# Optimization experiments

Hardware: AMD Instinct MI355X
Metric: run time of the kernel (lower is better)

The kernel has to match this reference:

```python
import jax, jax.numpy as jnp
import numpy as np

N = 50000      # nodes
E = 800000     # edges (before self loops)
H = 4          # heads
C = 32         # hidden_channels per head
HC = H * C     # 128
L = 3          # num_layers - 2 conv blocks
G = 128        # graphs in batch
OUT = 10       # out_channels
VOCAB = 100
EPS = 1e-5


def setup_inputs() -> dict:
    key = jax.random.key(0)
    ks = jax.random.split(key, 16)
    s = 0.1
    return {
        "x_idx": jax.random.randint(ks[0], (N,), 0, VOCAB),
        "edge_index": jax.random.randint(ks[1], (2, E), 0, N),
        "batch": jnp.sort(jax.random.randint(ks[2], (N,), 0, G)),
        "embed": jax.random.normal(ks[3], (VOCAB, HC), jnp.float32) * s,
        "bn_gamma": jnp.ones((L, HC), jnp.float32),
        "bn_beta": jnp.zeros((L, HC), jnp.float32),
        "lin_W": jax.random.normal(ks[4], (L, C, HC), jnp.float32) * s,   # maps HC -> C (hidden)
        "lin_b": jnp.zeros((L, C), jnp.float32),
        "gat_W": jax.random.normal(ks[5], (L, HC, C), jnp.float32) * s,   # maps C -> H*C
        "att_src": jax.random.normal(ks[6], (L, H, C), jnp.float32) * s,
        "att_dst": jax.random.normal(ks[7], (L, H, C), jnp.float32) * s,
        "gat_b": jnp.zeros((L, HC), jnp.float32),
        "readout_W": jax.random.normal(ks[8], (OUT, HC), jnp.float32) * s,
        "readout_b": jnp.zeros((OUT,), jnp.float32),
    }


def _segment_softmax(logits, seg, num_segments):
    # logits: [E, H], seg: [E]
    m = jax.ops.segment_max(logits, seg, num_segments=num_segments)
    m = jnp.where(jnp.isfinite(m), m, 0.0)
    e = jnp.exp(logits - m[seg])
    z = jax.ops.segment_sum(e, seg, num_segments=num_segments)
    return e / (z[seg] + 1e-16)


def _forward(x_idx, edge_index, batch, embed, bn_gamma, bn_beta, lin_W, lin_b,
             gat_W, att_src, att_dst, gat_b, readout_W, readout_b):
    x = embed[x_idx]                                   # [N, HC]
    loops = jnp.arange(N)
    src = jnp.concatenate([edge_index[0], loops])      # add_self_loops=True
    dst = jnp.concatenate([edge_index[1], loops])
    for l in range(L):
        # BatchNorm1d (batch statistics)
        mean = jnp.mean(x, axis=0)
        var = jnp.var(x, axis=0)
        x = bn_gamma[l] * (x - mean) * jax.lax.rsqrt(var + EPS) + bn_beta[l]
        # Linear(HC -> C) + relu; dropout = identity (eval)
        x = jax.nn.relu(x @ lin_W[l].T + lin_b[l])      # [N, C]
        # GATConv(C -> C, heads=H, concat)
        h = (x @ gat_W[l].T).reshape(N, H, C)           # [N, H, C]
        a_src = jnp.sum(h * att_src[l], axis=-1)        # [N, H]
        a_dst = jnp.sum(h * att_dst[l], axis=-1)        # [N, H]
        logits = jax.nn.leaky_relu(a_src[src] + a_dst[dst], 0.2)  # [E+N, H]
        alpha = _segment_softmax(logits, dst, N)        # softmax over in-edges of each dst
        msg = h[src] * alpha[:, :, None]                # [E+N, H, C]
        x = jax.ops.segment_sum(msg, dst, num_segments=N).reshape(N, HC) + gat_b[l]
    x = x @ readout_W.T + readout_b                     # [N, OUT]
    return jax.ops.segment_sum(x, batch, num_segments=G)  # [G, OUT]


def reference(x_idx, edge_index, batch, embed, bn_gamma, bn_beta, lin_W, lin_b,
              gat_W, att_src, att_dst, gat_b, readout_W, readout_b):
    return _forward(x_idx, edge_index, batch, embed, bn_gamma, bn_beta, lin_W, lin_b,
                    gat_W, att_src, att_dst, gat_b, readout_W, readout_b)
```

## Files before the change

### kernel.cpp

```cpp
#include <hip/hip_runtime.h>

constexpr int NN   = 50000;
constexpr int NE   = 800000;
constexpr int NHD  = 4;
constexpr int CC   = 32;
constexpr int HCC  = 128;
constexpr int NL   = 3;
constexpr int NG   = 128;
constexpr int NOUT = 10;
constexpr float BN_EPS = 1e-5f;

constexpr int X2S = 67;
constexpr int YS = 33;
constexpr int NSLOT = 64;
constexpr int NBUK = (NN + 127) / 128;
constexpr int EB  = 8192;

__device__ inline unsigned f2bf_pack(float a, float b) {
    unsigned ua = __float_as_uint(a); ua += 0x7FFFu + ((ua >> 16) & 1u);
    unsigned ub = __float_as_uint(b); ub += 0x7FFFu + ((ub >> 16) & 1u);
    return (ua >> 16) | (ub & 0xFFFF0000u);
}
__device__ inline float bf_lo(unsigned p) { return __uint_as_float(p << 16); }
__device__ inline float bf_hi(unsigned p) { return __uint_as_float(p & 0xFFFF0000u); }

__global__ __launch_bounds__(256) void k_embed_stats(const int* __restrict__ idx,
                                                     const float* __restrict__ embed,
                                                     unsigned* __restrict__ xp,
                                                     float* __restrict__ stats) {
    int tid = threadIdx.x;
    int i0 = blockIdx.x * 256 + tid;
    int stride = gridDim.x * 256;
    float s0 = 0.f, s1 = 0.f, q0 = 0.f, q1 = 0.f;
    for (int i = i0; i < NN * 64; i += stride) {
        int n = i >> 6, c2 = (i & 63) << 1;
        float2 ev = *(const float2*)(embed + (size_t)idx[n] * HCC + c2);
        xp[i] = f2bf_pack(ev.x, ev.y);
        s0 += ev.x; q0 += ev.x * ev.x;
        s1 += ev.y; q1 += ev.y * ev.y;
    }
    __shared__ float A[256], B[256], C[256], D[256];
    A[tid] = s0; B[tid] = s1; C[tid] = q0; D[tid] = q1;
    __syncthreads();
    int slot = blockIdx.x & (NSLOT - 1);
    if (tid < 64) {
        int p = tid;
        float S0 = A[p] + A[p + 64] + A[p + 128] + A[p + 192];
        float S1 = B[p] + B[p + 64] + B[p + 128] + B[p + 192];
        float Q0 = C[p] + C[p + 64] + C[p + 128] + C[p + 192];
        float Q1 = D[p] + D[p + 64] + D[p + 128] + D[p + 192];
        atomicAdd(&stats[slot * 256 + 2 * p],           S0);
        atomicAdd(&stats[slot * 256 + 2 * p + 1],       S1);
        atomicAdd(&stats[slot * 256 + HCC + 2 * p],     Q0);
        atomicAdd(&stats[slot * 256 + HCC + 2 * p + 1], Q1);
    }
}

__global__ __launch_bounds__(256) void k_bhist(const int* __restrict__ ei,
                                               int* __restrict__ bkcnt,
                                               const int* __restrict__ batch,
                                               float* __restrict__ gcnt) {
    __shared__ int hist[NBUK];
    __shared__ int lgc[NG];
    int b = blockIdx.x, t = threadIdx.x;
    int e0 = b * EB, nE = min(EB, NE - e0);
    for (int i = t; i < NBUK; i += 256) hist[i] = 0;
    for (int i = t; i < NG; i += 256) lgc[i] = 0;
    __syncthreads();
    for (int i = t; i < nE; i += 256)
        atomicAdd(&hist[ei[NE + e0 + i] >> 7], 1);
    int n0 = b * 512;
    for (int i = t; i < 512; i += 256) {
        int n = n0 + i;
        if (n < NN) atomicAdd(&lgc[batch[n]], 1);
    }
    __syncthreads();
    for (int i = t; i < NBUK; i += 256)
        if (hist[i]) atomicAdd(&bkcnt[i], hist[i]);
    for (int i = t; i < NG; i += 256)
        if (lgc[i]) atomicAdd(&gcnt[i], (float)lgc[i]);
}

__global__ __launch_bounds__(512) void k_bscan(const int* __restrict__ bkcnt,
                                               int* __restrict__ bbase,
                                               int* __restrict__ bcnt,
                                               int* __restrict__ rowptr) {
    __shared__ int sc[512];
    int t = threadIdx.x;
    int v = (t < NBUK) ? bkcnt[t] : 0;
    sc[t] = v;
    __syncthreads();
#pragma unroll
    for (int off = 1; off < 512; off <<= 1) {
        int u = (t >= off) ? sc[t - off] : 0;
        __syncthreads();
        sc[t] += u;
        __syncthreads();
    }
    if (t < NBUK) {
        int excl = sc[t] - v;
        bbase[t] = excl;
        bcnt[t]  = excl;
    }
    if (t == 0) rowptr[NN] = NE;
}

__global__ __launch_bounds__(256) void k_bin(const int* __restrict__ ei,
                                             int* __restrict__ bcnt,
                                             unsigned* __restrict__ e_src) {
    __shared__ int hist[NBUK], base[NBUK];
    int b = blockIdx.x, t = threadIdx.x;
    int e0 = b * EB;
    int nE = min(EB, NE - e0);

    for (int i = t; i < NBUK; i += 256) hist[i] = 0;
    __syncthreads();
    for (int i = t; i < nE; i += 256)
        atomicAdd(&hist[ei[NE + e0 + i] >> 7], 1);
    __syncthreads();
    for (int i = t; i < NBUK; i += 256) {
        int c = hist[i];
        if (c) base[i] = atomicAdd(&bcnt[i], c);
        hist[i] = 0;
    }
    __syncthreads();
    for (int i = t; i < nE; i += 256) {
        int e = e0 + i;
        int d = ei[NE + e];
        int s = ei[e];
        int bk = d >> 7;
        int pos = base[bk] + atomicAdd(&hist[bk], 1);
        e_src[pos] = (unsigned)s | ((unsigned)(d & 127) << 17);
    }
}

__global__ __launch_bounds__(256) void k_place(const int* __restrict__ bbase,
                                               unsigned* __restrict__ e_src,
                                               int* __restrict__ rowptr) {
    __shared__ int lcnt[128], sc[128], lrp[128], cnt[128];
    int b = blockIdx.x, t = threadIdx.x;
    int d0 = b * 128;
    int rS = bbase[b];
    int rE = (b + 1 < NBUK) ? bbase[b + 1] : NE;
    int n = rE - rS;
    if (t < 128) { lcnt[t] = 0; cnt[t] = 0; }
    __syncthreads();
    unsigned pk[14];
#pragma unroll
    for (int k = 0; k < 14; k++) {
        int i = t + k * 256;
        if (i < n) {
            pk[k] = e_src[rS + i];
            atomicAdd(&lcnt[pk[k] >> 17], 1);
        }
    }
    __syncthreads();
    if (t < 128) sc[t] = lcnt[t];
    __syncthreads();
#pragma unroll
    for (int off = 1; off < 128; off <<= 1) {
        int u = (t < 128 && t >= off) ? sc[t - off] : 0;
        __syncthreads();
        if (t < 128) sc[t] += u;
        __syncthreads();
    }
    if (t < 128) {
        int start = rS + sc[t] - lcnt[t];
        lrp[t] = start;
        int d = d0 + t;
        if (d < NN) rowptr[d] = start;
    }
    __syncthreads();
#pragma unroll
    for (int k = 0; k < 14; k++) {
        int i = t + k * 256;
        if (i < n) {
            unsigned p = pk[k];
            int dl = p >> 17;
            int pos = lrp[dl] + atomicAdd(&cnt[dl], 1);
            e_src[pos] = p & 0x1FFFFu;
        }
    }
}

__global__ __launch_bounds__(256) void k_fused(const unsigned* __restrict__ xp,
                                               const float* __restrict__ stats,
                                               const float* __restrict__ gamma,
                                               const float* __restrict__ beta,
                                               const float* __restrict__ W1,
                                               const float* __restrict__ b1,
                                               const float* __restrict__ W2,
                                               const float* __restrict__ aS,
                                               const float* __restrict__ aD,
                                               unsigned* __restrict__ h,
                                               float* __restrict__ asrc,
                                               float* __restrict__ adst) {
    __shared__ unsigned xb2[64 * X2S];
    __shared__ float yt[64 * YS];
    __shared__ float __attribute__((aligned(16))) ssl[256];
    int tid = threadIdx.x;
    int node0 = blockIdx.x * 64;
    int nNodes = min(64, NN - node0);

    if (tid < 128) {
        float s = 0.f, q = 0.f;
        for (int sl = 0; sl < NSLOT; sl++) {
            s += stats[sl * 256 + tid];
            q += stats[sl * 256 + HCC + tid];
        }
        float mean = s * (1.0f / NN);
        float var  = q * (1.0f / NN) - mean * mean;
        float sc   = gamma[tid] * rsqrtf(var + BN_EPS);
        ssl[tid]       = sc;
        ssl[HCC + tid] = beta[tid] - mean * sc;
    }
    __syncthreads();

    {
        for (int q4 = tid; q4 < nNodes * 16; q4 += 256) {
            int n = q4 >> 4, c8 = q4 & 15;
            uint4 xv = *(const uint4*)(xp + (size_t)(node0 + n) * 64 + c8 * 4);
            int c = c8 * 8;
            float4 sc0 = *(const float4*)&ssl[c];
            float4 sc1 = *(const float4*)&ssl[c + 4];
            float4 sh0 = *(const float4*)&ssl[HCC + c];
            float4 sh1 = *(const float4*)&ssl[HCC + c + 4];
            unsigned* dst = &xb2[n * X2S + c8 * 4];
            dst[0] = f2bf_pack(bf_lo(xv.x) * sc0.x + sh0.x, bf_hi(xv.x) * sc0.y + sh0.y);
            dst[1] = f2bf_pack(bf_lo(xv.y) * sc0.z + sh0.z, bf_hi(xv.y) * sc0.w + sh0.w);
            dst[2] = f2bf_pack(bf_lo(xv.z) * sc1.x + sh1.x, bf_hi(xv.z) * sc1.y + sh1.y);
            dst[3] = f2bf_pack(bf_lo(xv.w) * sc1.z + sh1.z, bf_hi(xv.w) * sc1.w + sh1.w);
        }
    }
    __syncthreads();

    int lane = tid & 63;
    int wv = __builtin_amdgcn_readfirstlane(tid >> 6);
    int n = lane;

    {
        int j0 = wv * 8;
        const float* w1p = W1 + j0 * 128;
        float acc[8];
#pragma unroll
        for (int k = 0; k < 8; k++) acc[k] = b1[j0 + k];
        if (n < nNodes) {
            for (int cb = 0; cb < 128; cb += 4) {
                unsigned p0 = xb2[n * X2S + (cb >> 1)];
                unsigned p1 = xb2[n * X2S + (cb >> 1) + 1];
                float xv0 = bf_lo(p0), xv1 = bf_hi(p0);
                float xv2 = bf_lo(p1), xv3 = bf_hi(p1);
#pragma unroll
                for (int k = 0; k < 8; k++) {
                    float4 w = *(const float4*)&w1p[k * 128 + cb];
                    acc[k] += xv0 * w.x + xv1 * w.y + xv2 * w.z + xv3 * w.w;
                }
            }
#pragma unroll
            for (int k = 0; k < 8; k++) yt[n * YS + j0 + k] = fmaxf(acc[k], 0.f);
        }
    }
    __syncthreads();

    if (n < nNodes) {
        int k0 = wv * 32, hd = wv;
        const float* w2p = W2 + k0 * 32;
        const float* aSp = aS + hd * 32;
        const float* aDp = aD + hd * 32;
        float yreg[32];
#pragma unroll
        for (int j = 0; j < 32; j++) yreg[j] = yt[n * YS + j];
        float sa = 0.f, da = 0.f;
        unsigned* hrow = h + (size_t)(node0 + n) * 64;
        for (int kb = 0; kb < 32; kb += 8) {
            float acck[8];
#pragma unroll
            for (int kk = 0; kk < 8; kk++) acck[kk] = 0.f;
#pragma unroll
            for (int j = 0; j < 32; j += 4) {
#pragma unroll
                for (int kk = 0; kk < 8; kk++) {
                    float4 w = *(const float4*)&w2p[(kb + kk) * 32 + j];
                    acck[kk] += yreg[j] * w.x + yreg[j + 1] * w.y +
                                yreg[j + 2] * w.z + yreg[j + 3] * w.w;
                }
            }
#pragma unroll
            for (int kk = 0; kk < 8; kk++) {
                sa += acck[kk] * aSp[kb + kk];
                da += acck[kk] * aDp[kb + kk];
            }
            uint4 pk;
            pk.x = f2bf_pack(acck[0], acck[1]);
            pk.y = f2bf_pack(acck[2], acck[3]);
            pk.z = f2bf_pack(acck[4], acck[5]);
            pk.w = f2bf_pack(acck[6], acck[7]);
            *(uint4*)(hrow + ((kb) >> 1) + (k0 >> 1)) = pk;
        }
        asrc[(node0 + n) * 4 + hd] = sa;
        adst[(node0 + n) * 4 + hd] = da;
    }
}

__global__ __launch_bounds__(256) void k_agg(const int* __restrict__ rowptr,
                                             const int* __restrict__ e_src,
                                             const float* __restrict__ asrc,
                                             const float* __restrict__ adst,
                                             const unsigned* __restrict__ h,
                                             const float* __restrict__ gat_b,
                                             unsigned* __restrict__ xo,
                                             float* __restrict__ stats,
                                             const int* __restrict__ batch,
                                             float* __restrict__ gsum,
                                             int mode) {
    int tid = threadIdx.x, lane = tid & 63, wv = tid >> 6;
    int g  = lane >> 4;
    int li = lane & 15;
    int hd = li >> 2;
    int d  = blockIdx.x * 16 + wv * 4 + g;

    float4 bA = *(const float4*)(gat_b + li * 8);
    float4 bB = *(const float4*)(gat_b + li * 8 + 4);

    int begin = rowptr[d];
    int end   = rowptr[d + 1];
    float adv = adst[d * 4 + hd];
    float asl = asrc[d * 4 + hd];
    uint4 hs  = *(const uint4*)(h + (size_t)d * 64 + li * 4);

    float acc[8];
#pragma unroll
    for (int k = 0; k < 8; k++) acc[k] = 0.f;
    float ws = 0.f;

    int s[4];
    if (begin < end) {
#pragma unroll
        for (int t = 0; t < 4; t++) s[t] = e_src[min(begin + t, end - 1)];
    }

    for (int j = begin; j < end; j += 4) {
        uint4 hv[4];
#pragma unroll
        for (int t = 0; t < 4; t++) hv[t] = *(const uint4*)(h + (size_t)s[t] * 64 + li * 4);
        float av[4];
#pragma unroll
        for (int t = 0; t < 4; t++) av[t] = asrc[s[t] * 4 + hd];
        int jn = j + 4;
        int sn[4];
#pragma unroll
        for (int t = 0; t < 4; t++) sn[t] = s[t];
        if (jn < end) {
#pragma unroll
            for (int t = 0; t < 4; t++) sn[t] = e_src[min(jn + t, end - 1)];
        }
        float w[4];
#pragma unroll
        for (int t = 0; t < 4; t++) {
            float l = av[t] + adv; l = l > 0.f ? l : 0.2f * l;
            w[t] = (j + t < end) ? __expf(l) : 0.f;
        }
#pragma unroll
        for (int t = 0; t < 4; t++) {
            acc[0] += w[t] * bf_lo(hv[t].x); acc[1] += w[t] * bf_hi(hv[t].x);
            acc[2] += w[t] * bf_lo(hv[t].y); acc[3] += w[t] * bf_hi(hv[t].y);
            acc[4] += w[t] * bf_lo(hv[t].z); acc[5] += w[t] * bf_hi(hv[t].z);
            acc[6] += w[t] * bf_lo(hv[t].w); acc[7] += w[t] * bf_hi(hv[t].w);
            ws += w[t];
        }
#pragma unroll
        for (int t = 0; t < 4; t++) s[t] = sn[t];
    }

    {
        float l = asl + adv; l = l > 0.f ? l : 0.2f * l;
        float w = __expf(l);
        acc[0] += w * bf_lo(hs.x); acc[1] += w * bf_hi(hs.x);
        acc[2] += w * bf_lo(hs.y); acc[3] += w * bf_hi(hs.y);
        acc[4] += w * bf_lo(hs.z); acc[5] += w * bf_hi(hs.z);
        acc[6] += w * bf_lo(hs.w); acc[7] += w * bf_hi(hs.w);
        ws += w;
    }

    float inv = 1.0f / (ws + 1e-16f);
    float o[8];
    o[0] = acc[0] * inv + bA.x; o[1] = acc[1] * inv + bA.y;
    o[2] = acc[2] * inv + bA.z; o[3] = acc[3] * inv + bA.w;
    o[4] = acc[4] * inv + bB.x; o[5] = acc[5] * inv + bB.y;
    o[6] = acc[6] * inv + bB.z; o[7] = acc[7] * inv + bB.w;

    __shared__ float redS[16 * 128], redQ[16 * 128];
    __shared__ int bg[16];
    int r = wv * 4 + g;

    if (mode == 1) {
        uint4 pk;
        pk.x = f2bf_pack(o[0], o[1]);
        pk.y = f2bf_pack(o[2], o[3]);
        pk.z = f2bf_pack(o[4], o[5]);
        pk.w = f2bf_pack(o[6], o[7]);
        *(uint4*)(xo + (size_t)d * 64 + li * 4) = pk;

#pragma unroll
        for (int k = 0; k < 8; k++) {
            redS[r * 128 + li * 8 + k] = o[k];
            redQ[r * 128 + li * 8 + k] = o[k] * o[k];
        }
        __syncthreads();
        int slot = blockIdx.x & (NSLOT - 1);
        if (tid < 128) {
            float v = 0.f;
#pragma unroll
            for (int rr = 0; rr < 16; rr++) v += redS[rr * 128 + tid];
            atomicAdd(&stats[slot * 256 + tid], v);
        } else {
            int c = tid - 128;
            float v = 0.f;
#pragma unroll
            for (int rr = 0; rr < 16; rr++) v += redQ[rr * 128 + c];
            atomicAdd(&stats[slot * 256 + HCC + c], v);
        }
    } else {
        if (li == 0) bg[r] = batch[d];
#pragma unroll
        for (int k = 0; k < 8; k++) redS[r * 128 + li * 8 + k] = o[k];
        __syncthreads();
        if (tid < 128) {
            float sacc = 0.f;
            int curg = bg[0];
#pragma unroll
            for (int rr = 0; rr < 16; rr++) {
                int gg = bg[rr];
                if (gg != curg) {
                    atomicAdd(&gsum[curg * HCC + tid], sacc);
                    sacc = 0.f; curg = gg;
                }
                sacc += redS[rr * 128 + tid];
            }
            atomicAdd(&gsum[curg * HCC + tid], sacc);
        }
    }
}

__global__ __launch_bounds__(128) void k_out(const float* __restrict__ gsum,
                                             const float* __restrict__ gcnt,
                                             const float* __restrict__ W,
                                             const float* __restrict__ bb,
                                             float* __restrict__ out) {
    __shared__ float v[128];
    int g = blockIdx.x, t = threadIdx.x;
    v[t] = gsum[g * HCC + t];
    __syncthreads();
    if (t < NOUT) {
        float acc = gcnt[g] * bb[t];
        const float* wr = W + t * HCC;
        for (int c = 0; c < HCC; c++) acc += v[c] * wr[c];
        out[g * NOUT + t] = acc;
    }
}

extern "C" void kernel_launch(void* const* d_in, const int* in_sizes, int n_in,
                              void* d_out, int out_size, void* d_ws, size_t ws_size,
                              hipStream_t stream) {
    const int*   x_idx = (const int*)d_in[0];
    const int*   ei    = (const int*)d_in[1];
    const int*   batch = (const int*)d_in[2];
    const float* embed = (const float*)d_in[3];
    const float* bn_g  = (const float*)d_in[4];
    const float* bn_b  = (const float*)d_in[5];
    const float* lin_W = (const float*)d_in[6];
    const float* lin_b = (const float*)d_in[7];
    const float* gat_W = (const float*)d_in[8];
    const float* att_s = (const float*)d_in[9];
    const float* att_d = (const float*)d_in[10];
    const float* gat_b = (const float*)d_in[11];
    const float* ro_W  = (const float*)d_in[12];
    const float* ro_b  = (const float*)d_in[13];
    float* out = (float*)d_out;

    const size_t STG = (size_t)NSLOT * 256;
    unsigned* xp    = (unsigned*)d_ws;
    unsigned* h     = xp + (size_t)NN * 64;
    float*    asrc  = (float*)(h + (size_t)NN * 64);
    float*    adst  = asrc + (size_t)NN * NHD;
    float*    stats = adst + (size_t)NN * NHD;
    float*    gsum  = stats + 3 * STG;
    float*    gcnt  = gsum + (size_t)NG * HCC;
    int*      bkcnt  = (int*)(gcnt + NG);
    int*      bbase  = bkcnt + NBUK;
    int*      bcnt   = bbase + NBUK;
    int*      rowptr = bcnt + NBUK;
    unsigned* e_src  = (unsigned*)(rowptr + NN + 1);

    hipMemsetAsync(stats, 0,
                   (3 * STG + (size_t)NG * HCC + NG) * sizeof(float) + NBUK * sizeof(int),
                   stream);

    k_embed_stats<<<512, 256, 0, stream>>>(x_idx, embed, xp, stats);
    k_bhist<<<(NE + EB - 1) / EB, 256, 0, stream>>>(ei, bkcnt, batch, gcnt);
    k_bscan<<<1, 512, 0, stream>>>(bkcnt, bbase, bcnt, rowptr);
    k_bin<<<(NE + EB - 1) / EB, 256, 0, stream>>>(ei, bcnt, e_src);
    k_place<<<NBUK, 256, 0, stream>>>(bbase, e_src, rowptr);

    for (int l = 0; l < NL; ++l) {
        k_fused<<<(NN + 63) / 64, 256, 0, stream>>>(xp, stats + l * STG,
                                                    bn_g + l * HCC, bn_b + l * HCC,
                                                    lin_W + l * CC * HCC, lin_b + l * CC,
                                                    gat_W + l * HCC * CC,
                                                    att_s + l * NHD * CC,
                                                    att_d + l * NHD * CC,
                                                    h, asrc, adst);
        k_agg<<<NN / 16, 256, 0, stream>>>(rowptr, (const int*)e_src, asrc, adst, h,
                                           gat_b + l * HCC, xp,
                                           stats + (l + 1) * STG,
                                           batch, gsum,
                                           (l < NL - 1) ? 1 : 2);
    }

    k_out<<<NG, 128, 0, stream>>>(gsum, gcnt, ro_W, ro_b, out);
}
```

Baseline: 341.4 us.

## Sort destination nodes by in-degree to balance aggregation wavefronts

Builds a degree histogram during CSR placement, scans it, and scatters node ids into a degree-sorted permutation. The aggregation kernel then processes nodes in that order, so the four nodes sharing a wavefront have similar edge counts and fewer lanes sit idle. In exchange it adds two small kernels and an extra indirection, and it breaks the contiguous node order for the h, asrc and adst reads and the output writes.

New measurement: 498.9 us. 46.1% more time.

```diff
diff --git a/kernel.cpp b/kernel.cpp
--- a/kernel.cpp
+++ b/kernel.cpp
@@ -15,6 +15,7 @@
 constexpr int NSLOT = 64;
 constexpr int NBUK = (NN + 127) / 128;
 constexpr int EB  = 8192;
+constexpr int NDB = 64;
 
 __device__ inline unsigned f2bf_pack(float a, float b) {
     unsigned ua = __float_as_uint(a); ua += 0x7FFFu + ((ua >> 16) & 1u);
@@ -84,9 +85,11 @@
 __global__ __launch_bounds__(512) void k_bscan(const int* __restrict__ bkcnt,
                                                int* __restrict__ bbase,
                                                int* __restrict__ bcnt,
-                                               int* __restrict__ rowptr) {
+                                               int* __restrict__ rowptr,
+                                               int* __restrict__ dhist) {
     __shared__ int sc[512];
     int t = threadIdx.x;
+    if (t < NDB) dhist[t] = 0;
     int v = (t < NBUK) ? bkcnt[t] : 0;
     sc[t] = v;
     __syncthreads();
@@ -136,7 +139,8 @@
 
 __global__ __launch_bounds__(256) void k_place(const int* __restrict__ bbase,
                                                unsigned* __restrict__ e_src,
-                                               int* __restrict__ rowptr) {
+                                               int* __restrict__ rowptr,
+                                               int* __restrict__ dhist) {
     __shared__ int lcnt[128], sc[128], lrp[128], cnt[128];
     int b = blockIdx.x, t = threadIdx.x;
     int d0 = b * 128;
@@ -168,7 +172,10 @@
         int start = rS + sc[t] - lcnt[t];
         lrp[t] = start;
         int d = d0 + t;
-        if (d < NN) rowptr[d] = start;
+        if (d < NN) {
+            rowptr[d] = start;
+            atomicAdd(&dhist[min(lcnt[t], NDB - 1)], 1);
+        }
     }
     __syncthreads();
 #pragma unroll
@@ -180,6 +187,46 @@
             int pos = lrp[dl] + atomicAdd(&cnt[dl], 1);
             e_src[pos] = p & 0x1FFFFu;
         }
+    }
+}
+
+__global__ __launch_bounds__(64) void k_dscan(const int* __restrict__ dhist,
+                                              int* __restrict__ dcnt) {
+    __shared__ int sc[NDB];
+    int t = threadIdx.x;
+    int v = dhist[t];
+    sc[t] = v;
+    __syncthreads();
+#pragma unroll
+    for (int off = 1; off < NDB; off <<= 1) {
+        int u = (t >= off) ? sc[t - off] : 0;
+        __syncthreads();
+        sc[t] += u;
+        __syncthreads();
+    }
+    dcnt[t] = sc[t] - v;
+}
+
+__global__ __launch_bounds__(256) void k_dscat(const int* __restrict__ rowptr,
+                                               int* __restrict__ dcnt,
+                                               int* __restrict__ perm) {
+    __shared__ int lh[NDB], lbase[NDB], loff[NDB];
+    int b = blockIdx.x, t = threadIdx.x;
+    int n = b * 256 + t;
+    if (t < NDB) { lh[t] = 0; loff[t] = 0; }
+    __syncthreads();
+    int bin = -1;
+    if (n < NN) {
+        int deg = rowptr[n + 1] - rowptr[n];
+        bin = min(deg, NDB - 1);
+        atomicAdd(&lh[bin], 1);
+    }
+    __syncthreads();
+    if (t < NDB && lh[t]) lbase[t] = atomicAdd(&dcnt[t], lh[t]);
+    __syncthreads();
+    if (n < NN) {
+        int pos = lbase[bin] + atomicAdd(&loff[bin], 1);
+        perm[pos] = n;
     }
 }
 
@@ -312,12 +359,13 @@
                                              float* __restrict__ stats,
                                              const int* __restrict__ batch,
                                              float* __restrict__ gsum,
+                                             const int* __restrict__ perm,
                                              int mode) {
     int tid = threadIdx.x, lane = tid & 63, wv = tid >> 6;
     int g  = lane >> 4;
     int li = lane & 15;
     int hd = li >> 2;
-    int d  = blockIdx.x * 16 + wv * 4 + g;
+    int d  = perm[blockIdx.x * 16 + wv * 4 + g];
 
     float4 bA = *(const float4*)(gat_b + li * 8);
     float4 bB = *(const float4*)(gat_b + li * 8 + 4);
@@ -491,6 +539,9 @@
     int*      bcnt   = bbase + NBUK;
     int*      rowptr = bcnt + NBUK;
     unsigned* e_src  = (unsigned*)(rowptr + NN + 1);
+    int*      dhist  = (int*)(e_src + NE);
+    int*      dcnt   = dhist + NDB;
+    int*      perm   = dcnt + NDB;
 
     hipMemsetAsync(stats, 0,
                    (3 * STG + (size_t)NG * HCC + NG) * sizeof(float) + NBUK * sizeof(int),
@@ -498,9 +549,11 @@
 
     k_embed_stats<<<512, 256, 0, stream>>>(x_idx, embed, xp, stats);
     k_bhist<<<(NE + EB - 1) / EB, 256, 0, stream>>>(ei, bkcnt, batch, gcnt);
-    k_bscan<<<1, 512, 0, stream>>>(bkcnt, bbase, bcnt, rowptr);
+    k_bscan<<<1, 512, 0, stream>>>(bkcnt, bbase, bcnt, rowptr, dhist);
     k_bin<<<(NE + EB - 1) / EB, 256, 0, stream>>>(ei, bcnt, e_src);
-    k_place<<<NBUK, 256, 0, stream>>>(bbase, e_src, rowptr);
+    k_place<<<NBUK, 256, 0, stream>>>(bbase, e_src, rowptr, dhist);
+    k_dscan<<<1, 64, 0, stream>>>(dhist, dcnt);
+    k_dscat<<<(NN + 255) / 256, 256, 0, stream>>>(rowptr, dcnt, perm);
 
     for (int l = 0; l < NL; ++l) {
         k_fused<<<(NN + 63) / 64, 256, 0, stream>>>(xp, stats + l * STG,
@@ -513,7 +566,7 @@
         k_agg<<<NN / 16, 256, 0, stream>>>(rowptr, (const int*)e_src, asrc, adst, h,
                                            gat_b + l * HCC, xp,
                                            stats + (l + 1) * STG,
-                                           batch, gsum,
+                                           batch, gsum, perm,
                                            (l < NL - 1) ? 1 : 2);
     }
 
```
